# Kernel optimization log

Hardware: AMD Instinct MI355X
Metric: run time of the kernel (lower is better)

The kernel has to match this reference:

```python
import jax, jax.numpy as jnp
import numpy as np
from jax import lax

B, S, H, V, P = 4, 512, 768, 30522, 512
EPS = 1e-12

def _layer_norm(x, gamma, beta):
    mu = jnp.mean(x, axis=-1, keepdims=True)
    var = jnp.mean(jnp.square(x - mu), axis=-1, keepdims=True)
    return (x - mu) * lax.rsqrt(var + EPS) * gamma + beta

def setup_inputs() -> dict:
    key = jax.random.key(0)
    ks = jax.random.split(key, 8)
    s = 0.02
    hidden_states = jax.random.normal(ks[0], (B, S, H), jnp.float32)
    # values in {-1, 0}; (span_mask > -1) marks in-span positions
    span_mask = jax.random.randint(ks[1], (B, S), -1, 1, dtype=jnp.int64)
    pos_emb = jax.random.normal(ks[2], (P, H), jnp.float32) * s
    W1 = jax.random.normal(ks[3], (3 * H, H), jnp.float32) * s
    b1 = jnp.zeros((H,), jnp.float32)
    g1 = jnp.ones((H,), jnp.float32)
    be1 = jnp.zeros((H,), jnp.float32)
    W2 = jax.random.normal(ks[4], (H, H), jnp.float32) * s
    b2 = jnp.zeros((H,), jnp.float32)
    g2 = jnp.ones((H,), jnp.float32)
    be2 = jnp.zeros((H,), jnp.float32)
    Wdec = jax.random.normal(ks[5], (H, V), jnp.float32) * s
    dec_bias = jnp.zeros((V,), jnp.float32)
    return {"hidden_states": hidden_states, "span_mask": span_mask, "pos_emb": pos_emb,
            "W1": W1, "b1": b1, "g1": g1, "be1": be1,
            "W2": W2, "b2": b2, "g2": g2, "be2": be2,
            "Wdec": Wdec, "dec_bias": dec_bias}

def reference(hidden_states, span_mask, pos_emb, W1, b1, g1, be1, W2, b2, g2, be2, Wdec, dec_bias):
    mask = span_mask > -1                       # [B,S] bool
    idx = jnp.arange(S, dtype=jnp.int64)
    # position embeddings via default position_ids = arange(S)
    pe = jnp.broadcast_to(pos_emb[:S][None], (B, S, H))
    # fw recurrence: fw[j] = j-1 if (mask[j] & ~mask[j-1]) else fw[j-1]; fw[0]=0
    prev = jnp.pad(mask[:, :-1], ((0, 0), (1, 0)))
    start = mask & ~prev & (idx > 0)[None]
    c_fw = jnp.where(start, idx - 1, 0)
    fw = lax.cummax(c_fw, axis=1)               # last span-start index (parallel max-scan)
    # bw recurrence: bw[j] = j+1 if (mask[j] & ~mask[j+1]) else bw[j+1]; bw[S-1]=S-1
    nxt = jnp.pad(mask[:, 1:], ((0, 0), (0, 1)))
    end = mask & ~nxt & (idx < S - 1)[None]
    c_bw = jnp.where(end, idx + 1, S - 1)
    bw = lax.cummin(c_bw, axis=1, reverse=True)  # nearest span-end index (reverse min-scan)
    fw_h = jnp.take_along_axis(hidden_states, fw[:, :, None], axis=1)  # [B,S,H]
    bw_h = jnp.take_along_axis(hidden_states, bw[:, :, None], axis=1)
    sbo = jnp.concatenate([fw_h, bw_h, pe], axis=-1)                   # [B,S,3H]
    sbo = sbo * mask[:, :, None].astype(sbo.dtype)
    mid = _layer_norm(jax.nn.gelu(sbo @ W1 + b1, approximate=False).astype(jnp.float32), g1, be1)
    pre = _layer_norm(jax.nn.gelu(mid @ W2 + b2, approximate=False).astype(jnp.float32), g2, be2)
    logits = pre @ Wdec + dec_bias                                     # [B,S,V]
    return logits
```

## Files before the change

kernel.cpp:

```cpp
#include <hip/hip_runtime.h>
#include <hip/hip_bf16.h>

#define BSZ 4
#define SEQ 512
#define HID 768
#define VOC 30522
#define NPAD 30720

typedef __attribute__((ext_vector_type(8))) short short8;
typedef __attribute__((ext_vector_type(4))) float f32x4;

typedef const unsigned int __attribute__((address_space(1)))* gptr_t;
typedef unsigned int __attribute__((address_space(3)))* lptr_t;

__device__ __forceinline__ void gload_lds16(const void* g, void* l) {
    __builtin_amdgcn_global_load_lds((gptr_t)g, (lptr_t)l, 16, 0, 0);
}

__global__ __launch_bounds__(512) void scan_kernel(const int* __restrict__ span,
                                                   int* __restrict__ fw, int* __restrict__ bw) {
    int b = blockIdx.x;
    int j = threadIdx.x;
    __shared__ int sm[SEQ];
    __shared__ int sc[SEQ];
    int m = (span[b * SEQ + j] > -1) ? 1 : 0;
    sm[j] = m;
    __syncthreads();
    int prev = (j > 0) ? sm[j - 1] : 0;
    int nxt  = (j < SEQ - 1) ? sm[j + 1] : 0;
    int cfw = (m && !prev && j > 0) ? (j - 1) : 0;
    int cbw = (m && !nxt && j < SEQ - 1) ? (j + 1) : (SEQ - 1);

    int v = cfw;
    sc[j] = v; __syncthreads();
    for (int off = 1; off < SEQ; off <<= 1) {
        int o = (j >= off) ? sc[j - off] : 0;
        __syncthreads();
        v = max(v, o);
        sc[j] = v; __syncthreads();
    }
    fw[b * SEQ + j] = v;

    v = cbw;
    sc[j] = v; __syncthreads();
    for (int off = 1; off < SEQ; off <<= 1) {
        int o = (j + off < SEQ) ? sc[j + off] : (SEQ - 1);
        __syncthreads();
        v = min(v, o);
        sc[j] = v; __syncthreads();
    }
    bw[b * SEQ + j] = v;
}

__global__ __launch_bounds__(256) void build_x(const float* __restrict__ h,
                                               const int* __restrict__ span,
                                               const float* __restrict__ pe,
                                               const int* __restrict__ fw,
                                               const int* __restrict__ bw,
                                               __hip_bfloat16* __restrict__ X) {
    int r = blockIdx.x;
    int b = r >> 9, s = r & (SEQ - 1);
    float mf = (span[r] > -1) ? 1.f : 0.f;
    int f = fw[r], w = bw[r];
    const float* hf = h + ((size_t)b * SEQ + f) * HID;
    const float* hb = h + ((size_t)b * SEQ + w) * HID;
    const float* pp = pe + (size_t)s * HID;
    __hip_bfloat16* xr = X + (size_t)r * (3 * HID);
    for (int c = threadIdx.x; c < HID; c += 256) {
        xr[c]            = __float2bfloat16(hf[c] * mf);
        xr[HID + c]      = __float2bfloat16(hb[c] * mf);
        xr[2 * HID + c]  = __float2bfloat16(pp[c] * mf);
    }
}

__global__ __launch_bounds__(256) void transpose64(const float* __restrict__ W,
                                                   __hip_bfloat16* __restrict__ Wt,
                                                   int K, int N) {
    __shared__ float t[64][67];
    int n0 = blockIdx.x * 64, k0 = blockIdx.y * 64;
    int tx = threadIdx.x & 31, ty = threadIdx.x >> 5;
    #pragma unroll
    for (int i = 0; i < 64; i += 8) {
        #pragma unroll
        for (int jx = 0; jx < 64; jx += 32) {
            int k = k0 + ty + i, n = n0 + tx + jx;
            t[ty + i][tx + jx] = (n < N) ? W[(size_t)k * N + n] : 0.f;
        }
    }
    __syncthreads();
    #pragma unroll
    for (int i = 0; i < 8; i++) {
        int nn = ty + i * 8;
        int n = n0 + nn;
        float a = t[tx * 2][nn], b = t[tx * 2 + 1][nn];
        __hip_bfloat16 ba = __float2bfloat16(a), bb = __float2bfloat16(b);
        unsigned int pk = ((unsigned int)*(unsigned short*)&bb << 16) | *(unsigned short*)&ba;
        *(unsigned int*)&Wt[(size_t)n * K + k0 + tx * 2] = pk;
    }
}

__global__ __launch_bounds__(256) void gelu_ln(const float* __restrict__ Y1,
                                               const float* __restrict__ Y2,
                                               const float* __restrict__ bias,
                                               const float* __restrict__ g,
                                               const float* __restrict__ be,
                                               __hip_bfloat16* __restrict__ out) {
    int r = blockIdx.x;
    const float* y1 = Y1 + (size_t)r * HID;
    const float* y2 = Y2 + (size_t)r * HID;
    float z[3];
    float s1 = 0.f, s2 = 0.f;
    #pragma unroll
    for (int i = 0; i < 3; i++) {
        int c = threadIdx.x + i * 256;
        float x = y1[c] + y2[c] + bias[c];
        float zz = 0.5f * x * (1.f + erff(x * 0.70710678118654752f));
        z[i] = zz; s1 += zz; s2 += zz * zz;
    }
    #pragma unroll
    for (int off = 32; off; off >>= 1) {
        s1 += __shfl_down(s1, off);
        s2 += __shfl_down(s2, off);
    }
    __shared__ float p1[4], p2[4];
    int w = threadIdx.x >> 6, lane = threadIdx.x & 63;
    if (lane == 0) { p1[w] = s1; p2[w] = s2; }
    __syncthreads();
    s1 = p1[0] + p1[1] + p1[2] + p1[3];
    s2 = p2[0] + p2[1] + p2[2] + p2[3];
    float mu = s1 * (1.f / HID);
    float var = s2 * (1.f / HID) - mu * mu;
    float rs = rsqrtf(var + 1e-12f);
    __hip_bfloat16* o = out + (size_t)r * HID;
    #pragma unroll
    for (int i = 0; i < 3; i++) {
        int c = threadIdx.x + i * 256;
        o[c] = __float2bfloat16((z[i] - mu) * rs * g[c] + be[c]);
    }
}

__global__ __launch_bounds__(256) void gemm_splitk(const __hip_bfloat16* __restrict__ A,
                                                   const __hip_bfloat16* __restrict__ Bt,
                                                   float* __restrict__ C,
                                                   int lda, int Klen, int ldc, size_t cstride) {
    __shared__ __hip_bfloat16 As[128 * 64];
    __shared__ __hip_bfloat16 Bs[128 * 64];
    int bx = blockIdx.x;
    int by = blockIdx.y;
    int koff = blockIdx.z * Klen;
    float* Cz = C + (size_t)blockIdx.z * cstride;
    int t = threadIdx.x;
    int lane = t & 63, w = t >> 6;
    int wm = w >> 1, wn = w & 1;

    const __hip_bfloat16* Ab = A + (size_t)(by * 128) * lda + koff;
    const __hip_bfloat16* Bb = Bt + (size_t)(bx * 128) * lda + koff;

    f32x4 acc[4][4] = {};

    for (int k0 = 0; k0 < Klen; k0 += 64) {
        #pragma unroll
        for (int i = 0; i < 4; i++) {
            int c = i * 256 + t;
            int row = c >> 3, col = (c & 7) * 8;
            gload_lds16(Ab + (size_t)row * lda + k0 + col, (char*)As + c * 16);
            gload_lds16(Bb + (size_t)row * lda + k0 + col, (char*)Bs + c * 16);
        }
        __syncthreads();
        #pragma unroll
        for (int kk = 0; kk < 64; kk += 32) {
            short8 a[4], b[4];
            int col = kk + (lane >> 4) * 8;
            #pragma unroll
            for (int mi = 0; mi < 4; mi++) {
                int row = wm * 64 + mi * 16 + (lane & 15);
                a[mi] = *(const short8*)&As[row * 64 + col];
            }
            #pragma unroll
            for (int ni = 0; ni < 4; ni++) {
                int row = wn * 64 + ni * 16 + (lane & 15);
                b[ni] = *(const short8*)&Bs[row * 64 + col];
            }
            #pragma unroll
            for (int mi = 0; mi < 4; mi++)
                #pragma unroll
                for (int ni = 0; ni < 4; ni++)
                    acc[mi][ni] = __builtin_amdgcn_mfma_f32_16x16x32_bf16(a[mi], b[ni], acc[mi][ni], 0, 0, 0);
        }
        __syncthreads();
    }

    int rq = lane >> 4, cl = lane & 15;
    #pragma unroll
    for (int mi = 0; mi < 4; mi++) {
        #pragma unroll
        for (int ni = 0; ni < 4; ni++) {
            int col = bx * 128 + wn * 64 + ni * 16 + cl;
            #pragma unroll
            for (int j = 0; j < 4; j++) {
                int row = by * 128 + wm * 64 + mi * 16 + rq * 4 + j;
                Cz[(size_t)row * ldc + col] = acc[mi][ni][j];
            }
        }
    }
}

#define KTILES 12
#define TPB 4
#define VTOT (KTILES * TPB)
__global__ __launch_bounds__(512, 2) void gemm256p(const __hip_bfloat16* __restrict__ A,
                                                   const __hip_bfloat16* __restrict__ Bt,
                                                   float* __restrict__ C,
                                                   int K, int Nvalid,
                                                   const float* __restrict__ bias, int ldc) {
    __shared__ char lds[131072];
    int h = blockIdx.x;
    int chunk = gridDim.x >> 3;
    int l = (h & 7) * chunk + (h >> 3);
    int bn = l >> 1;
    int bm0 = (l & 1) * 4;

    int tid = threadIdx.x;
    int lane = tid & 63;
    int w = tid >> 6;
    int wr = w >> 2, wc = w & 3;

    int r0 = tid >> 3;
    int swz8 = (((tid & 7) ^ (r0 & 7)) << 3);
    const __hip_bfloat16* Bbase = Bt + (size_t)(bn * 256) * K;
    size_t arow0 = (size_t)r0 * K + swz8;
    size_t arow1 = arow0 + (size_t)64 * K;
    int ldsw = tid * 16;

    int rxor = (lane & 7) << 4;
    int rcol = ((lane >> 4) & 3) * 16;
    int rc0 = (0 + rcol) ^ rxor;
    int rc1 = (64 + rcol) ^ rxor;
    int aoff = (wr * 64 + (lane & 15)) * 128;
    int boff = 32768 + (wc * 32 + (lane & 15)) * 128;

    int rq = lane >> 4, cl = lane & 15;
    float bv[2][2];
    #pragma unroll
    for (int qn = 0; qn < 2; qn++)
        #pragma unroll
        for (int ni = 0; ni < 2; ni++) {
            int col = bn * 256 + qn * 128 + wc * 32 + ni * 16 + cl;
            bv[qn][ni] = (col < Nvalid) ? bias[col] : 0.f;
        }

    f32x4 acc[2][2][4][2] = {};

#define ABASE(va) (A + (size_t)((bm0 + (va) / KTILES) * 256) * K)
#define KKOF(va)  (((va) % KTILES) * 64)
#define STAGEA(va, half) do { \
        const __hip_bfloat16* gg = ABASE(va) + (size_t)(half) * 128 * K + KKOF(va); \
        char* dd = lds + ((va) & 1) * 65536 + (half) * 16384 + ldsw; \
        gload_lds16(gg + arow0, dd); \
        gload_lds16(gg + arow1, dd + 8192); } while (0)
#define STAGEB(va, half) do { \
        const __hip_bfloat16* gg = Bbase + (size_t)(half) * 128 * K + KKOF(va); \
        char* dd = lds + ((va) & 1) * 65536 + 32768 + (half) * 16384 + ldsw; \
        gload_lds16(gg + arow0, dd); \
        gload_lds16(gg + arow1, dd + 8192); } while (0)

#define MFMA_Q(qm, qn, AF, BF) do { \
        _Pragma("unroll") \
        for (int mi = 0; mi < 4; mi++) \
            _Pragma("unroll") \
            for (int ni = 0; ni < 2; ni++) { \
                acc[qm][qn][mi][ni] = __builtin_amdgcn_mfma_f32_16x16x32_bf16(AF[mi][0], BF[ni][0], acc[qm][qn][mi][ni], 0, 0, 0); \
                acc[qm][qn][mi][ni] = __builtin_amdgcn_mfma_f32_16x16x32_bf16(AF[mi][1], BF[ni][1], acc[qm][qn][mi][ni], 0, 0, 0); \
            } } while (0)

#define WRQ(qm, qn) do { \
        int bmw = bm0 + v / KTILES; \
        _Pragma("unroll") \
        for (int mi = 0; mi < 4; mi++) \
            _Pragma("unroll") \
            for (int ni = 0; ni < 2; ni++) { \
                int col = bn * 256 + (qn) * 128 + wc * 32 + ni * 16 + cl; \
                if (col < Nvalid) { \
                    _Pragma("unroll") \
                    for (int j = 0; j < 4; j++) { \
                        int row = bmw * 256 + (qm) * 128 + wr * 64 + mi * 16 + rq * 4 + j; \
                        C[(size_t)row * ldc + col] = acc[qm][qn][mi][ni][j] + bv[qn][ni]; \
                    } \
                } \
                acc[qm][qn][mi][ni] = (f32x4){0.f, 0.f, 0.f, 0.f}; \
            } } while (0)

#define BAR() __builtin_amdgcn_s_barrier()

    STAGEA(0, 0); STAGEB(0, 0); STAGEB(0, 1); STAGEA(0, 1);
    STAGEA(1, 0); STAGEB(1, 0); STAGEB(1, 1);
    asm volatile("s_waitcnt vmcnt(6)" ::: "memory");
    BAR();

    short8 af0[4][2], af1[4][2], bf0[2][2], bf1[2][2];
    for (int v = 0; v < VTOT; ++v) {
        int d = (v & 1) * 65536;
        bool last = ((v % KTILES) == KTILES - 1);

        #pragma unroll
        for (int mi = 0; mi < 4; mi++) {
            af0[mi][0] = *(const short8*)(lds + d + aoff + mi * 2048 + rc0);
            af0[mi][1] = *(const short8*)(lds + d + aoff + mi * 2048 + rc1);
        }
        #pragma unroll
        for (int ni = 0; ni < 2; ni++) {
            bf0[ni][0] = *(const short8*)(lds + d + boff + ni * 2048 + rc0);
            bf0[ni][1] = *(const short8*)(lds + d + boff + ni * 2048 + rc1);
        }
        if (v + 1 < VTOT) STAGEA(v + 1, 1);
        BAR();
        __builtin_amdgcn_s_setprio(1);
        MFMA_Q(0, 0, af0, bf0);
        __builtin_amdgcn_s_setprio(0);
        if (last) WRQ(0, 0);
        BAR();

        #pragma unroll
        for (int ni = 0; ni < 2; ni++) {
            bf1[ni][0] = *(const short8*)(lds + d + boff + 16384 + ni * 2048 + rc0);
            bf1[ni][1] = *(const short8*)(lds + d + boff + 16384 + ni * 2048 + rc1);
        }
        if (v + 2 < VTOT) STAGEA(v + 2, 0);
        BAR();
        __builtin_amdgcn_s_setprio(1);
        MFMA_Q(0, 1, af0, bf1);
        __builtin_amdgcn_s_setprio(0);
        if (last) WRQ(0, 1);
        BAR();

        #pragma unroll
        for (int mi = 0; mi < 4; mi++) {
            af1[mi][0] = *(const short8*)(lds + d + 16384 + aoff + mi * 2048 + rc0);
            af1[mi][1] = *(const short8*)(lds + d + 16384 + aoff + mi * 2048 + rc1);
        }
        if (v + 2 < VTOT) STAGEB(v + 2, 0);
        BAR();
        __builtin_amdgcn_s_setprio(1);
        MFMA_Q(1, 1, af1, bf1);
        __builtin_amdgcn_s_setprio(0);
        if (last) WRQ(1, 1);
        BAR();

        if (v + 2 < VTOT) STAGEB(v + 2, 1);
        if (v < VTOT - 2) asm volatile("s_waitcnt vmcnt(6)" ::: "memory");
        else              asm volatile("s_waitcnt vmcnt(0)" ::: "memory");
        BAR();
        __builtin_amdgcn_s_setprio(1);
        MFMA_Q(1, 0, af1, bf0);
        __builtin_amdgcn_s_setprio(0);
        if (last) WRQ(1, 0);
        BAR();
    }
#undef STAGEA
#undef STAGEB
#undef MFMA_Q
#undef WRQ
#undef BAR
#undef ABASE
#undef KKOF
}

extern "C" void kernel_launch(void* const* d_in, const int* in_sizes, int n_in,
                              void* d_out, int out_size, void* d_ws, size_t ws_size,
                              hipStream_t stream) {
    const float* hidden = (const float*)d_in[0];
    const int*   span   = (const int*)d_in[1];
    const float* pe     = (const float*)d_in[2];
    const float* W1     = (const float*)d_in[3];
    const float* b1     = (const float*)d_in[4];
    const float* g1     = (const float*)d_in[5];
    const float* be1    = (const float*)d_in[6];
    const float* W2     = (const float*)d_in[7];
    const float* b2     = (const float*)d_in[8];
    const float* g2     = (const float*)d_in[9];
    const float* be2    = (const float*)d_in[10];
    const float* Wdec   = (const float*)d_in[11];
    const float* dbias  = (const float*)d_in[12];
    float* out = (float*)d_out;

    const int M = BSZ * SEQ;
    char* ws = (char*)d_ws;
    size_t off = 0;
    int* fw = (int*)(ws + off);                 off += (size_t)M * 4;
    int* bw = (int*)(ws + off);                 off += (size_t)M * 4;
    __hip_bfloat16* Xb   = (__hip_bfloat16*)(ws + off); off += (size_t)M * 3 * HID * 2;
    __hip_bfloat16* W1t  = (__hip_bfloat16*)(ws + off); off += (size_t)HID * 3 * HID * 2;
    __hip_bfloat16* W2t  = (__hip_bfloat16*)(ws + off); off += (size_t)HID * HID * 2;
    __hip_bfloat16* Wdt  = (__hip_bfloat16*)(ws + off); off += (size_t)NPAD * HID * 2;
    float* Y             = (float*)(ws + off);          off += (size_t)M * HID * 4 * 2;
    __hip_bfloat16* mid  = (__hip_bfloat16*)(ws + off); off += (size_t)M * HID * 2;
    __hip_bfloat16* pre  = (__hip_bfloat16*)(ws + off); off += (size_t)M * HID * 2;
    float* Y2 = Y + (size_t)M * HID;

    scan_kernel<<<BSZ, SEQ, 0, stream>>>(span, fw, bw);
    build_x<<<M, 256, 0, stream>>>(hidden, span, pe, fw, bw, Xb);
    transpose64<<<dim3(HID / 64, 3 * HID / 64), 256, 0, stream>>>(W1, W1t, 3 * HID, HID);
    transpose64<<<dim3(HID / 64, HID / 64), 256, 0, stream>>>(W2, W2t, HID, HID);
    transpose64<<<dim3(NPAD / 64, HID / 64), 256, 0, stream>>>(Wdec, Wdt, HID, VOC);
    gemm_splitk<<<dim3(HID / 128, M / 128, 2), 256, 0, stream>>>(Xb, W1t, Y, 3 * HID, 3 * HID / 2, HID, (size_t)M * HID);
    gelu_ln<<<M, 256, 0, stream>>>(Y, Y2, b1, g1, be1, mid);
    gemm_splitk<<<dim3(HID / 128, M / 128, 2), 256, 0, stream>>>(mid, W2t, Y, HID, HID / 2, HID, (size_t)M * HID);
    gelu_ln<<<M, 256, 0, stream>>>(Y, Y2, b2, g2, be2, pre);
    gemm256p<<<240, 512, 0, stream>>>(pre, Wdt, out, HID, VOC, dbias, VOC);
}
```

Baseline: 253.0 us.

## Merge weight transposes, vectorize build_x, and raise split-K for first GEMM

```diff
diff --git a/kernel.cpp b/kernel.cpp
--- a/kernel.cpp
+++ b/kernel.cpp
@@ -52,7 +52,7 @@
     bw[b * SEQ + j] = v;
 }
 
-__global__ __launch_bounds__(256) void build_x(const float* __restrict__ h,
+__global__ __launch_bounds__(384) void build_x(const float* __restrict__ h,
                                                const int* __restrict__ span,
                                                const float* __restrict__ pe,
                                                const int* __restrict__ fw,
@@ -66,18 +66,32 @@
     const float* hb = h + ((size_t)b * SEQ + w) * HID;
     const float* pp = pe + (size_t)s * HID;
     __hip_bfloat16* xr = X + (size_t)r * (3 * HID);
-    for (int c = threadIdx.x; c < HID; c += 256) {
-        xr[c]            = __float2bfloat16(hf[c] * mf);
-        xr[HID + c]      = __float2bfloat16(hb[c] * mf);
-        xr[2 * HID + c]  = __float2bfloat16(pp[c] * mf);
-    }
-}
-
-__global__ __launch_bounds__(256) void transpose64(const float* __restrict__ W,
-                                                   __hip_bfloat16* __restrict__ Wt,
-                                                   int K, int N) {
+    int c = threadIdx.x * 2;
+    #pragma unroll
+    for (int seg = 0; seg < 3; seg++) {
+        const float* src = (seg == 0) ? hf : (seg == 1) ? hb : pp;
+        float2 v = *(const float2*)&src[c];
+        __hip_bfloat16 lo = __float2bfloat16(v.x * mf);
+        __hip_bfloat16 hi = __float2bfloat16(v.y * mf);
+        unsigned int pk = ((unsigned int)*(unsigned short*)&hi << 16) | *(unsigned short*)&lo;
+        *(unsigned int*)&xr[seg * HID + c] = pk;
+    }
+}
+
+#define T1_TILES (12 * 36)
+#define T2_TILES (12 * 12)
+#define TD_TILES (480 * 12)
+__global__ __launch_bounds__(256) void transpose_all(const float* __restrict__ W1, __hip_bfloat16* __restrict__ W1t,
+                                                     const float* __restrict__ W2, __hip_bfloat16* __restrict__ W2t,
+                                                     const float* __restrict__ Wd, __hip_bfloat16* __restrict__ Wdt) {
+    int flat = blockIdx.x;
+    const float* W; __hip_bfloat16* Wt; int K, N, tx_tiles, idx;
+    if (flat < T1_TILES)                { W = W1; Wt = W1t; K = 3 * HID; N = HID; tx_tiles = 12;  idx = flat; }
+    else if (flat < T1_TILES + T2_TILES){ W = W2; Wt = W2t; K = HID;     N = HID; tx_tiles = 12;  idx = flat - T1_TILES; }
+    else                                { W = Wd; Wt = Wdt; K = HID;     N = VOC; tx_tiles = 480; idx = flat - T1_TILES - T2_TILES; }
+    int n0 = (idx % tx_tiles) * 64, k0 = (idx / tx_tiles) * 64;
+
     __shared__ float t[64][67];
-    int n0 = blockIdx.x * 64, k0 = blockIdx.y * 64;
     int tx = threadIdx.x & 31, ty = threadIdx.x >> 5;
     #pragma unroll
     for (int i = 0; i < 64; i += 8) {
@@ -99,21 +113,22 @@
     }
 }
 
-__global__ __launch_bounds__(256) void gelu_ln(const float* __restrict__ Y1,
-                                               const float* __restrict__ Y2,
+template<int P>
+__global__ __launch_bounds__(256) void gelu_ln(const float* __restrict__ Y, size_t ystride,
                                                const float* __restrict__ bias,
                                                const float* __restrict__ g,
                                                const float* __restrict__ be,
                                                __hip_bfloat16* __restrict__ out) {
     int r = blockIdx.x;
-    const float* y1 = Y1 + (size_t)r * HID;
-    const float* y2 = Y2 + (size_t)r * HID;
     float z[3];
     float s1 = 0.f, s2 = 0.f;
     #pragma unroll
     for (int i = 0; i < 3; i++) {
         int c = threadIdx.x + i * 256;
-        float x = y1[c] + y2[c] + bias[c];
+        float x = bias[c];
+        #pragma unroll
+        for (int p = 0; p < P; p++)
+            x += Y[p * ystride + (size_t)r * HID + c];
         float zz = 0.5f * x * (1.f + erff(x * 0.70710678118654752f));
         z[i] = zz; s1 += zz; s2 += zz * zz;
     }
@@ -392,19 +407,17 @@
     __hip_bfloat16* W1t  = (__hip_bfloat16*)(ws + off); off += (size_t)HID * 3 * HID * 2;
     __hip_bfloat16* W2t  = (__hip_bfloat16*)(ws + off); off += (size_t)HID * HID * 2;
     __hip_bfloat16* Wdt  = (__hip_bfloat16*)(ws + off); off += (size_t)NPAD * HID * 2;
-    float* Y             = (float*)(ws + off);          off += (size_t)M * HID * 4 * 2;
+    float* Y             = (float*)(ws + off);          off += (size_t)M * HID * 4 * 4;
     __hip_bfloat16* mid  = (__hip_bfloat16*)(ws + off); off += (size_t)M * HID * 2;
     __hip_bfloat16* pre  = (__hip_bfloat16*)(ws + off); off += (size_t)M * HID * 2;
-    float* Y2 = Y + (size_t)M * HID;
+    size_t ystride = (size_t)M * HID;
 
     scan_kernel<<<BSZ, SEQ, 0, stream>>>(span, fw, bw);
-    build_x<<<M, 256, 0, stream>>>(hidden, span, pe, fw, bw, Xb);
-    transpose64<<<dim3(HID / 64, 3 * HID / 64), 256, 0, stream>>>(W1, W1t, 3 * HID, HID);
-    transpose64<<<dim3(HID / 64, HID / 64), 256, 0, stream>>>(W2, W2t, HID, HID);
-    transpose64<<<dim3(NPAD / 64, HID / 64), 256, 0, stream>>>(Wdec, Wdt, HID, VOC);
-    gemm_splitk<<<dim3(HID / 128, M / 128, 2), 256, 0, stream>>>(Xb, W1t, Y, 3 * HID, 3 * HID / 2, HID, (size_t)M * HID);
-    gelu_ln<<<M, 256, 0, stream>>>(Y, Y2, b1, g1, be1, mid);
-    gemm_splitk<<<dim3(HID / 128, M / 128, 2), 256, 0, stream>>>(mid, W2t, Y, HID, HID / 2, HID, (size_t)M * HID);
-    gelu_ln<<<M, 256, 0, stream>>>(Y, Y2, b2, g2, be2, pre);
+    build_x<<<M, 384, 0, stream>>>(hidden, span, pe, fw, bw, Xb);
+    transpose_all<<<T1_TILES + T2_TILES + TD_TILES, 256, 0, stream>>>(W1, W1t, W2, W2t, Wdec, Wdt);
+    gemm_splitk<<<dim3(HID / 128, M / 128, 4), 256, 0, stream>>>(Xb, W1t, Y, 3 * HID, 3 * HID / 4, HID, ystride);
+    gelu_ln<4><<<M, 256, 0, stream>>>(Y, ystride, b1, g1, be1, mid);
+    gemm_splitk<<<dim3(HID / 128, M / 128, 2), 256, 0, stream>>>(mid, W2t, Y, HID, HID / 2, HID, ystride);
+    gelu_ln<2><<<M, 256, 0, stream>>>(Y, ystride, b2, g2, be2, pre);
     gemm256p<<<240, 512, 0, stream>>>(pre, Wdt, out, HID, VOC, dbias, VOC);
 }
```

Result: faster. 233.8 us (-7.6%).
